# Optimization experiments

Hardware: AMD Instinct MI355X
Metric: run time of the kernel (lower is better)

Reference implementation:

```python
import jax, jax.numpy as jnp
import numpy as np

B, T, D = 2, 4096, 768
H = 12
HD = D // H  # 64
SCALE = 1.0 / np.sqrt(HD)


def setup_inputs() -> dict:
    key = jax.random.key(0)
    k1, k2, k3 = jax.random.split(key, 3)
    x = jax.random.normal(k1, (B, T, D), dtype=jnp.float32)
    W_qkv = jax.random.normal(k2, (D, 3 * D), dtype=jnp.float32) * (1.0 / np.sqrt(D))
    b_qkv = jnp.zeros((3 * D,), dtype=jnp.float32)
    W_out = jax.random.normal(k3, (D, D), dtype=jnp.float32) * (1.0 / np.sqrt(D))
    b_out = jnp.zeros((D,), dtype=jnp.float32)
    return {"x": x, "W_qkv": W_qkv, "b_qkv": b_qkv, "W_out": W_out, "b_out": b_out}


def reference(x, W_qkv, b_qkv, W_out, b_out):
    Bx, Tx, C = x.shape
    qkv = x @ W_qkv + b_qkv                                  # [B,T,3D]
    qkv = qkv.reshape(Bx, Tx, 3, H, HD).transpose(2, 0, 3, 1, 4)  # [3,B,H,T,hd]
    q, k, v = qkv[0], qkv[1], qkv[2]
    scores = jnp.einsum('bhqd,bhkd->bhqk', q, k) * SCALE      # [B,H,T,T]
    causal = jnp.tril(jnp.ones((Tx, Tx), dtype=bool))
    scores = jnp.where(causal[None, None], scores, -jnp.inf)
    attn = jax.nn.softmax(scores, axis=-1)
    out = jnp.einsum('bhqk,bhkd->bhqd', attn, v)              # [B,H,T,hd]
    out = out.transpose(0, 2, 1, 3).reshape(Bx, Tx, C)        # [B,T,D]
    return out @ W_out + b_out
```

## Files before the change

### kernel.cpp

```cpp
#include <hip/hip_runtime.h>
#include <cstdint>
#include <cstddef>

typedef _Float16 f16x8 __attribute__((ext_vector_type(8)));
typedef _Float16 f16x4 __attribute__((ext_vector_type(4)));
typedef float    f32x4 __attribute__((ext_vector_type(4)));

#define AS_GLOBAL __attribute__((address_space(1)))
#define AS_LDS    __attribute__((address_space(3)))

__device__ __forceinline__ void load16_to_lds(const _Float16* g, _Float16* l) {
    __builtin_amdgcn_global_load_lds((const AS_GLOBAL void*)g, (AS_LDS void*)l, 16, 0, 0);
}

#define BB   2
#define TT   4096
#define DD   768
#define NH   12
#define HDIM 64
#define D3   2304
#define SC2  (0.125f * 1.44269504088896f)

__global__ __launch_bounds__(256) void prep(const float* __restrict__ x,
                                            _Float16* __restrict__ Xh,
                                            const float* __restrict__ Wqkv,
                                            _Float16* __restrict__ Wqkvt,
                                            const float* __restrict__ Wout,
                                            _Float16* __restrict__ Wot) {
    const int bid = blockIdx.x, tid = threadIdx.x;
    if (bid < 6144) {
        const int i = bid * 1024 + tid * 4;
        float4 v = *(const float4*)(x + i);
        f16x4 h;
        h[0] = (_Float16)v.x; h[1] = (_Float16)v.y;
        h[2] = (_Float16)v.z; h[3] = (_Float16)v.w;
        *(f16x4*)(Xh + i) = h;
        return;
    }
    __shared__ float tile[32][33];
    const float* in; _Float16* out; int C, bx, by;
    if (bid < 7872) {
        const int t = bid - 6144;
        in = Wqkv; out = Wqkvt; C = 2304;
        bx = (t % 72) * 32; by = (t / 72) * 32;
    } else {
        const int t = bid - 7872;
        in = Wout; out = Wot; C = 768;
        bx = (t % 24) * 32; by = (t / 24) * 32;
    }
    const int R = 768;
    const int tx = tid & 31, ty = tid >> 5;
#pragma unroll
    for (int j = 0; j < 32; j += 8)
        tile[ty + j][tx] = in[(size_t)(by + ty + j) * C + bx + tx];
    __syncthreads();
#pragma unroll
    for (int j = 0; j < 32; j += 8)
        out[(size_t)(bx + ty + j) * R + by + tx] = (_Float16)tile[tx][ty + j];
}

template <typename OutT>
__device__ __forceinline__ void gemm_body(const _Float16* __restrict__ A,
                                          const _Float16* __restrict__ Bt,
                                          const float* __restrict__ bias, bool bias_row,
                                          OutT* __restrict__ C, int N, int K,
                                          int m0, int n0,
                                          _Float16* As, _Float16* Bs) {
    const int tid  = threadIdx.x;
    const int wave = tid >> 6, lane = tid & 63, quad = lane >> 4, l16 = lane & 15;
    const int wm = (wave & 1) * 64, wn = (wave >> 1) * 64;
    const int rowc = lane >> 3, part = lane & 7;

    f32x4 acc[4][4];
#pragma unroll
    for (int i = 0; i < 4; ++i)
#pragma unroll
        for (int n = 0; n < 4; ++n) acc[i][n] = f32x4{0.f, 0.f, 0.f, 0.f};

    for (int k0 = 0; k0 < K; k0 += 64) {
        __syncthreads();
#pragma unroll
        for (int cc = 0; cc < 4; ++cc) {
            const int ch = wave * 4 + cc;
            load16_to_lds(A  + (size_t)(m0 + ch * 8 + rowc) * K + k0 + part * 8,
                          As + ch * 512);
            load16_to_lds(Bt + (size_t)(n0 + ch * 8 + rowc) * K + k0 + part * 8,
                          Bs + ch * 512);
        }
        __syncthreads();
#pragma unroll
        for (int i = 0; i < 4; ++i) {
            f16x8 a0 = *(const f16x8*)(As + (wm + i * 16 + l16) * 64 + quad * 8);
            f16x8 a1 = *(const f16x8*)(As + (wm + i * 16 + l16) * 64 + 32 + quad * 8);
#pragma unroll
            for (int n = 0; n < 4; ++n) {
                f16x8 b0 = *(const f16x8*)(Bs + (wn + n * 16 + l16) * 64 + quad * 8);
                f16x8 b1 = *(const f16x8*)(Bs + (wn + n * 16 + l16) * 64 + 32 + quad * 8);
                acc[i][n] = __builtin_amdgcn_mfma_f32_16x16x32_f16(a0, b0, acc[i][n], 0, 0, 0);
                acc[i][n] = __builtin_amdgcn_mfma_f32_16x16x32_f16(a1, b1, acc[i][n], 0, 0, 0);
            }
        }
    }
#pragma unroll
    for (int i = 0; i < 4; ++i)
#pragma unroll
        for (int n = 0; n < 4; ++n)
#pragma unroll
            for (int r = 0; r < 4; ++r) {
                const int row = m0 + wm + i * 16 + quad * 4 + r;
                const int col = n0 + wn + n * 16 + l16;
                const float bv = bias_row ? bias[row] : bias[col];
                C[(size_t)row * N + col] = (OutT)(acc[i][n][r] + bv);
            }
}

__global__ __launch_bounds__(256) void gemm_qkv(const _Float16* __restrict__ Xh,
                                                const _Float16* __restrict__ Wqkvt,
                                                const float* __restrict__ bqkv,
                                                _Float16* __restrict__ QKh,
                                                _Float16* __restrict__ VtG) {
    __shared__ __align__(16) _Float16 As[128 * 64];
    __shared__ __align__(16) _Float16 Bs[128 * 64];
    const int bid = blockIdx.x;
    if (bid < 768) {
        const int xcd = bid & 7, j = bid >> 3;
        const int by = xcd + 8 * (j / 12);
        const int bx = j % 12;
        gemm_body<_Float16>(Xh, Wqkvt, bqkv, false, QKh, 1536, DD,
                            by * 128, bx * 128, As, Bs);
    } else {
        const int t = bid - 768;
        const int xcd = t & 7, j = t >> 3;
        const int bx = xcd + 8 * (j / 6);
        const int by = j % 6;
        gemm_body<_Float16>(Wqkvt + (size_t)1536 * DD, Xh, bqkv + 1536, true, VtG,
                            8192, DD, by * 128, bx * 128, As, Bs);
    }
}

__global__ __launch_bounds__(256) void gemm_out(const _Float16* __restrict__ A,
                                                const _Float16* __restrict__ Bt,
                                                const float* __restrict__ bias,
                                                float* __restrict__ C) {
    __shared__ __align__(16) _Float16 As[64 * 64];
    __shared__ __align__(16) _Float16 Bs[128 * 64];
    const int L = blockIdx.x;
    const int xcd = L & 7, j = L >> 3;
    const int by = xcd + 8 * (j / 6);
    const int bx = j % 6;
    const int m0 = by * 64, n0 = bx * 128;
    const int N = DD, K = DD;
    const int tid  = threadIdx.x;
    const int wave = tid >> 6, lane = tid & 63, quad = lane >> 4, l16 = lane & 15;
    const int wm = (wave & 1) * 32, wn = (wave >> 1) * 64;
    const int rowc = lane >> 3, part = lane & 7;

    f32x4 acc[2][4];
#pragma unroll
    for (int i = 0; i < 2; ++i)
#pragma unroll
        for (int n = 0; n < 4; ++n) acc[i][n] = f32x4{0.f, 0.f, 0.f, 0.f};

    for (int k0 = 0; k0 < K; k0 += 64) {
        __syncthreads();
#pragma unroll
        for (int cc = 0; cc < 2; ++cc) {
            const int ch = wave * 2 + cc;
            load16_to_lds(A + (size_t)(m0 + ch * 8 + rowc) * K + k0 + part * 8,
                          As + ch * 512);
        }
#pragma unroll
        for (int cc = 0; cc < 4; ++cc) {
            const int ch = wave * 4 + cc;
            load16_to_lds(Bt + (size_t)(n0 + ch * 8 + rowc) * K + k0 + part * 8,
                          Bs + ch * 512);
        }
        __syncthreads();
#pragma unroll
        for (int i = 0; i < 2; ++i) {
            f16x8 a0 = *(const f16x8*)(As + (wm + i * 16 + l16) * 64 + quad * 8);
            f16x8 a1 = *(const f16x8*)(As + (wm + i * 16 + l16) * 64 + 32 + quad * 8);
#pragma unroll
            for (int n = 0; n < 4; ++n) {
                f16x8 b0 = *(const f16x8*)(Bs + (wn + n * 16 + l16) * 64 + quad * 8);
                f16x8 b1 = *(const f16x8*)(Bs + (wn + n * 16 + l16) * 64 + 32 + quad * 8);
                acc[i][n] = __builtin_amdgcn_mfma_f32_16x16x32_f16(a0, b0, acc[i][n], 0, 0, 0);
                acc[i][n] = __builtin_amdgcn_mfma_f32_16x16x32_f16(a1, b1, acc[i][n], 0, 0, 0);
            }
        }
    }
#pragma unroll
    for (int i = 0; i < 2; ++i)
#pragma unroll
        for (int n = 0; n < 4; ++n)
#pragma unroll
            for (int r = 0; r < 4; ++r) {
                const int row = m0 + wm + i * 16 + quad * 4 + r;
                const int col = n0 + wn + n * 16 + l16;
                C[(size_t)row * N + col] = acc[i][n][r] + bias[col];
            }
}

__global__ __launch_bounds__(256, 5) void attn_kernel(const _Float16* __restrict__ qk,
                                                      const _Float16* __restrict__ vt,
                                                      _Float16* __restrict__ ao) {
    __shared__ __align__(16) _Float16 Ks[2][64 * 64];
    __shared__ __align__(16) _Float16 Vs[2][64 * 64];

    const int L    = blockIdx.x;
    const int xcd  = L & 7;
    const int r_   = L >> 3;
    const int gIdx = r_ % 3;
    const int qt   = 63 - r_ / 3;
    const int g    = gIdx * 8 + xcd;
    const int b = g / NH, h = g % NH;

    const int tid = threadIdx.x;
    const int wave = tid >> 6, lane = tid & 63, quad = lane >> 4, l16 = lane & 15;
    const int wq = wave >> 1, wk = wave & 1;

    f16x4 ones4;
#pragma unroll
    for (int j = 0; j < 4; ++j) ones4[j] = (_Float16)1.0f;

    int vK[2], vV[2];
#pragma unroll
    for (int p = 0; p < 2; ++p) {
        const int j   = wave * 16 + p * 8 + (lane >> 3);
        const int cdk = (lane & 7) ^ (j & 7);
        vK[p] = (b * TT + j) * 1536 + DD + h * HDIM + cdk * 8;
        vV[p] = (h * HDIM + j) * 8192 + b * TT + cdk * 8;
    }
    auto stage = [&](int buf, int k0) {
        const int kK = k0 * 1536;
#pragma unroll
        for (int p = 0; p < 2; ++p) {
            load16_to_lds(qk + (vK[p] + kK), Ks[buf] + (wave * 16 + p * 8) * 64);
            load16_to_lds(vt + (vV[p] + k0), Vs[buf] + (wave * 16 + p * 8) * 64);
        }
    };

    const int q0 = qt * 64;
    const int nkt = qt + 1;
    const int qrow0 = q0 + wq * 32;
    const int qr_lane = qrow0 + l16;
    f16x8 aq[2][2];
#pragma unroll
    for (int mq = 0; mq < 2; ++mq) {
        const int qoff = (b * TT + qrow0 + mq * 16 + l16) * 1536 + h * HDIM + quad * 8;
        const _Float16 sc = (_Float16)SC2;
        aq[mq][0] = *(const f16x8*)(qk + qoff) * sc;
        aq[mq][1] = *(const f16x8*)(qk + qoff + 32) * sc;
    }
    f32x4 o[2][4], lac[2];
#pragma unroll
    for (int mq = 0; mq < 2; ++mq) {
#pragma unroll
        for (int n = 0; n < 4; ++n) o[mq][n] = f32x4{0.f, 0.f, 0.f, 0.f};
        lac[mq] = f32x4{0.f, 0.f, 0.f, 0.f};
    }

    stage(0, 0);
    int cur = 0;
    for (int kt = 0; kt < nkt; ++kt) {
        __syncthreads();
        if (kt + 1 < nkt) stage(cur ^ 1, (kt + 1) * 64);

        __builtin_amdgcn_s_setprio(1);
        f32x4 s[2][2];
#pragma unroll
        for (int mq = 0; mq < 2; ++mq)
#pragma unroll
            for (int n1 = 0; n1 < 2; ++n1) s[mq][n1] = f32x4{0.f, 0.f, 0.f, 0.f};
#pragma unroll
        for (int kh = 0; kh < 2; ++kh)
#pragma unroll
            for (int n1 = 0; n1 < 2; ++n1) {
                const int rowK = (wk * 2 + n1) * 16 + l16;
                const int pos = (kh * 4 + quad) ^ (l16 & 7);
                f16x8 bk = *(const f16x8*)(Ks[cur] + rowK * 64 + pos * 8);
                s[0][n1] = __builtin_amdgcn_mfma_f32_16x16x32_f16(bk, aq[0][kh], s[0][n1], 0, 0, 0);
                s[1][n1] = __builtin_amdgcn_mfma_f32_16x16x32_f16(bk, aq[1][kh], s[1][n1], 0, 0, 0);
            }
        __builtin_amdgcn_s_setprio(0);

        if (kt == nkt - 1) {
#pragma unroll
            for (int mq = 0; mq < 2; ++mq) {
                const int qr = qr_lane + mq * 16;
#pragma unroll
                for (int n1 = 0; n1 < 2; ++n1) {
                    const int kg0 = kt * 64 + wk * 32 + n1 * 16 + quad * 4;
#pragma unroll
                    for (int r = 0; r < 4; ++r)
                        if (kg0 + r > qr) s[mq][n1][r] = -1e30f;
                }
            }
        }

        f16x4 pa[2][2];
#pragma unroll
        for (int mq = 0; mq < 2; ++mq)
#pragma unroll
            for (int n1 = 0; n1 < 2; ++n1)
#pragma unroll
                for (int r = 0; r < 4; ++r)
                    pa[mq][n1][r] = (_Float16)__builtin_amdgcn_exp2f(s[mq][n1][r]);

        __builtin_amdgcn_s_setprio(1);
#pragma unroll
        for (int mq = 0; mq < 2; ++mq) {
            lac[mq] = __builtin_amdgcn_mfma_f32_16x16x16f16(pa[mq][0], ones4, lac[mq], 0, 0, 0);
            lac[mq] = __builtin_amdgcn_mfma_f32_16x16x16f16(pa[mq][1], ones4, lac[mq], 0, 0, 0);
        }
#pragma unroll
        for (int n1 = 0; n1 < 2; ++n1)
#pragma unroll
            for (int n = 0; n < 4; ++n) {
                const int rowV = n * 16 + l16;
                const int lc  = wk * 4 + n1 * 2 + (quad >> 1);
                const int pc  = lc ^ (l16 & 7);
                f16x4 bv = *(const f16x4*)(Vs[cur] + rowV * 64 + pc * 8 + (quad & 1) * 4);
                o[0][n] = __builtin_amdgcn_mfma_f32_16x16x16f16(pa[0][n1], bv, o[0][n], 0, 0, 0);
                o[1][n] = __builtin_amdgcn_mfma_f32_16x16x16f16(pa[1][n1], bv, o[1][n], 0, 0, 0);
            }
        __builtin_amdgcn_s_setprio(0);
        cur ^= 1;
    }

    __syncthreads();
    float* const Ksf = (float*)&Ks[0][0];
    float* const Vsf = (float*)&Vs[0][0];
    if (wk) {
#pragma unroll
        for (int mq = 0; mq < 2; ++mq) {
            if (l16 == 0)
                *(f32x4*)(Vsf + wq * 32 + mq * 16 + quad * 4) = lac[mq];
#pragma unroll
            for (int n = 0; n < 4; ++n)
                *(f32x4*)(Ksf + wq * 2048 + (mq * 4 + n) * 256 + lane * 4) = o[mq][n];
        }
    }
    __syncthreads();
    if (!wk) {
#pragma unroll
        for (int mq = 0; mq < 2; ++mq) {
            f32x4 lp = *(const f32x4*)(Vsf + wq * 32 + mq * 16 + quad * 4);
            f32x4 inv;
#pragma unroll
            for (int r = 0; r < 4; ++r) inv[r] = 1.0f / (lac[mq][r] + lp[r]);
#pragma unroll
            for (int n = 0; n < 4; ++n) {
                f32x4 op = *(const f32x4*)(Ksf + wq * 2048 + (mq * 4 + n) * 256 + lane * 4);
#pragma unroll
                for (int r = 0; r < 4; ++r) {
                    const int ooff = (b * TT + qrow0 + mq * 16 + quad * 4 + r) * DD + h * HDIM + l16;
                    ao[ooff + n * 16] = (_Float16)((o[mq][n][r] + op[r]) * inv[r]);
                }
            }
        }
    }
}

extern "C" void kernel_launch(void* const* d_in, const int* in_sizes, int n_in,
                              void* d_out, int out_size, void* d_ws, size_t ws_size,
                              hipStream_t stream) {
    const float* x     = (const float*)d_in[0];
    const float* Wqkv  = (const float*)d_in[1];
    const float* bqkv  = (const float*)d_in[2];
    const float* Wout  = (const float*)d_in[3];
    const float* bout  = (const float*)d_in[4];
    float* out = (float*)d_out;

    char* ws = (char*)d_ws;
    _Float16* Xh    = (_Float16*)ws;  ws += (size_t)BB * TT * DD * 2;
    _Float16* Wqkvt = (_Float16*)ws;  ws += (size_t)D3 * DD * 2;
    _Float16* Wot   = (_Float16*)ws;  ws += (size_t)DD * DD * 2;
    _Float16* QKh   = (_Float16*)ws;  ws += (size_t)BB * TT * 1536 * 2;
    _Float16* VtG   = (_Float16*)ws;  ws += (size_t)DD * BB * TT * 2;
    _Float16* AOh   = (_Float16*)ws;  ws += (size_t)BB * TT * DD * 2;

    prep<<<8448, 256, 0, stream>>>(x, Xh, Wqkv, Wqkvt, Wout, Wot);

    gemm_qkv<<<1152, 256, 0, stream>>>(Xh, Wqkvt, bqkv, QKh, VtG);

    attn_kernel<<<1536, 256, 0, stream>>>(QKh, VtG, AOh);

    gemm_out<<<768, 256, 0, stream>>>(AOh, Wot, bout, out);
}
```

Baseline: 239.0 us.

## Interleave QK and PV halves in attention loop and reswizzle V tile

Splits each key tile's work into two 16-column halves and software-pipelines them, so the exp of one half overlaps the QK MFMAs of the next half and the PV MFMAs of the previous one. Setprio regions are adjusted to match. It also changes the XOR swizzle used for the V tile in LDS (both the staging address and the read address) to a permuted row mapping, aiming to reduce bank conflicts on the 4-wide V reads. This adds scheduling complexity, and correctness depends on the store and load swizzles matching.

```diff
diff --git a/kernel.cpp b/kernel.cpp
--- a/kernel.cpp
+++ b/kernel.cpp
@@ -228,8 +228,9 @@
     for (int p = 0; p < 2; ++p) {
         const int j   = wave * 16 + p * 8 + (lane >> 3);
         const int cdk = (lane & 7) ^ (j & 7);
+        const int cdv = (lane & 7) ^ (((j & 3) << 1) | ((j >> 2) & 1));
         vK[p] = (b * TT + j) * 1536 + DD + h * HDIM + cdk * 8;
-        vV[p] = (h * HDIM + j) * 8192 + b * TT + cdk * 8;
+        vV[p] = (h * HDIM + j) * 8192 + b * TT + cdv * 8;
     }
     auto stage = [&](int buf, int k0) {
         const int kK = k0 * 1536;
@@ -244,6 +245,7 @@
     const int nkt = qt + 1;
     const int qrow0 = q0 + wq * 32;
     const int qr_lane = qrow0 + l16;
+    const int rv = ((l16 & 3) << 1) | ((l16 >> 2) & 1);
     f16x8 aq[2][2];
 #pragma unroll
     for (int mq = 0; mq < 2; ++mq) {
@@ -266,64 +268,69 @@
         __syncthreads();
         if (kt + 1 < nkt) stage(cur ^ 1, (kt + 1) * 64);
 
-        __builtin_amdgcn_s_setprio(1);
         f32x4 s[2][2];
+        f16x4 pa[2][2];
 #pragma unroll
         for (int mq = 0; mq < 2; ++mq)
 #pragma unroll
             for (int n1 = 0; n1 < 2; ++n1) s[mq][n1] = f32x4{0.f, 0.f, 0.f, 0.f};
-#pragma unroll
-        for (int kh = 0; kh < 2; ++kh)
-#pragma unroll
-            for (int n1 = 0; n1 < 2; ++n1) {
+
+        auto qk_half = [&](int n1) {
+#pragma unroll
+            for (int kh = 0; kh < 2; ++kh) {
                 const int rowK = (wk * 2 + n1) * 16 + l16;
                 const int pos = (kh * 4 + quad) ^ (l16 & 7);
                 f16x8 bk = *(const f16x8*)(Ks[cur] + rowK * 64 + pos * 8);
                 s[0][n1] = __builtin_amdgcn_mfma_f32_16x16x32_f16(bk, aq[0][kh], s[0][n1], 0, 0, 0);
                 s[1][n1] = __builtin_amdgcn_mfma_f32_16x16x32_f16(bk, aq[1][kh], s[1][n1], 0, 0, 0);
             }
-        __builtin_amdgcn_s_setprio(0);
-
-        if (kt == nkt - 1) {
+        };
+        auto mask_half = [&](int n1) {
 #pragma unroll
             for (int mq = 0; mq < 2; ++mq) {
                 const int qr = qr_lane + mq * 16;
-#pragma unroll
-                for (int n1 = 0; n1 < 2; ++n1) {
-                    const int kg0 = kt * 64 + wk * 32 + n1 * 16 + quad * 4;
-#pragma unroll
-                    for (int r = 0; r < 4; ++r)
-                        if (kg0 + r > qr) s[mq][n1][r] = -1e30f;
-                }
-            }
-        }
-
-        f16x4 pa[2][2];
-#pragma unroll
-        for (int mq = 0; mq < 2; ++mq)
-#pragma unroll
-            for (int n1 = 0; n1 < 2; ++n1)
+                const int kg0 = kt * 64 + wk * 32 + n1 * 16 + quad * 4;
+#pragma unroll
+                for (int r = 0; r < 4; ++r)
+                    if (kg0 + r > qr) s[mq][n1][r] = -1e30f;
+            }
+        };
+        auto exp_half = [&](int n1) {
+#pragma unroll
+            for (int mq = 0; mq < 2; ++mq)
 #pragma unroll
                 for (int r = 0; r < 4; ++r)
                     pa[mq][n1][r] = (_Float16)__builtin_amdgcn_exp2f(s[mq][n1][r]);
-
-        __builtin_amdgcn_s_setprio(1);
-#pragma unroll
-        for (int mq = 0; mq < 2; ++mq) {
-            lac[mq] = __builtin_amdgcn_mfma_f32_16x16x16f16(pa[mq][0], ones4, lac[mq], 0, 0, 0);
-            lac[mq] = __builtin_amdgcn_mfma_f32_16x16x16f16(pa[mq][1], ones4, lac[mq], 0, 0, 0);
-        }
-#pragma unroll
-        for (int n1 = 0; n1 < 2; ++n1)
+        };
+        auto pv_half = [&](int n1) {
+            f16x4 ap0 = pa[0][n1], ap1 = pa[1][n1];
+            lac[0] = __builtin_amdgcn_mfma_f32_16x16x16f16(ap0, ones4, lac[0], 0, 0, 0);
+            lac[1] = __builtin_amdgcn_mfma_f32_16x16x16f16(ap1, ones4, lac[1], 0, 0, 0);
 #pragma unroll
             for (int n = 0; n < 4; ++n) {
                 const int rowV = n * 16 + l16;
                 const int lc  = wk * 4 + n1 * 2 + (quad >> 1);
-                const int pc  = lc ^ (l16 & 7);
+                const int pc  = lc ^ rv;
                 f16x4 bv = *(const f16x4*)(Vs[cur] + rowV * 64 + pc * 8 + (quad & 1) * 4);
-                o[0][n] = __builtin_amdgcn_mfma_f32_16x16x16f16(pa[0][n1], bv, o[0][n], 0, 0, 0);
-                o[1][n] = __builtin_amdgcn_mfma_f32_16x16x16f16(pa[1][n1], bv, o[1][n], 0, 0, 0);
-            }
+                o[0][n] = __builtin_amdgcn_mfma_f32_16x16x16f16(ap0, bv, o[0][n], 0, 0, 0);
+                o[1][n] = __builtin_amdgcn_mfma_f32_16x16x16f16(ap1, bv, o[1][n], 0, 0, 0);
+            }
+        };
+
+        const bool last = (kt == nkt - 1);
+        __builtin_amdgcn_s_setprio(1);
+        qk_half(0);
+        __builtin_amdgcn_s_setprio(0);
+        if (last) mask_half(0);
+        exp_half(0);
+        __builtin_amdgcn_s_setprio(1);
+        qk_half(1);
+        pv_half(0);
+        __builtin_amdgcn_s_setprio(0);
+        if (last) mask_half(1);
+        exp_half(1);
+        __builtin_amdgcn_s_setprio(1);
+        pv_half(1);
         __builtin_amdgcn_s_setprio(0);
         cur ^= 1;
     }
```

Measured after the change: 234.8 us. No clear change (-1.7%).
